# Optimization experiments

Hardware: AMD Instinct MI355X
Metric: run time of the kernel (lower is better)

Reference implementation:

```python
import jax, jax.numpy as jnp
import numpy as np

B, T, F, H = 1024, 128, 128, 256


def setup_inputs() -> dict:
    key = jax.random.key(0)
    ks = jax.random.split(key, 13)
    u = lambda k, shape, std: jax.random.uniform(k, shape, jnp.float32, -std, std)
    sH = 1.0 / np.sqrt(H)
    sF = 1.0 / np.sqrt(F)
    return {
        "X": jax.random.normal(ks[0], (B, T, F), jnp.float32),
        "M": (jax.random.uniform(ks[1], (B, T, F)) > 0.5).astype(jnp.float32),
        "Delta": jax.random.uniform(ks[2], (B, T, F), jnp.float32),
        "mu": jax.random.normal(ks[3], (B, 1, F), jnp.float32),
        "X_locf": jax.random.normal(ks[4], (B, T, F), jnp.float32),
        # TemporalDecay decay_h: W [H, F], b [H]
        "Wdh": u(ks[5], (H, F), sH),
        "bdh": u(ks[6], (H,), sH),
        # TemporalDecay decay_x (diag): W [F, F], b [F] (only diagonal of W used)
        "Wdx": u(ks[7], (F, F), sF),
        "bdx": u(ks[8], (F,), sF),
        # GRUCell: input size 2F+H, hidden H
        "Wih": u(ks[9], (3 * H, 2 * F + H), sH),
        "Whh": u(ks[10], (3 * H, H), sH),
        "bih": u(ks[11], (3 * H,), sH),
        "bhh": u(ks[12], (3 * H,), sH),
    }


def reference(X, M, Delta, mu, X_locf, Wdh, bdh, Wdx, bdx, Wih, Whh, bih, bhh):
    diag_x = jnp.diagonal(Wdx)  # diag=True: F.linear(d, W*I) == d * diag(W)
    mu_b = mu[:, 0, :]  # [B, F]

    def step(h, xs):
        x_t, m_t, d_t, xl_t = xs  # each [B, F]
        gamma_h = jnp.exp(-jax.nn.relu(d_t @ Wdh.T + bdh))  # [B, H]
        gamma_x = jnp.exp(-jax.nn.relu(d_t * diag_x + bdx))  # [B, F]
        h = h * gamma_h
        rep = h  # appended BEFORE the GRU cell update
        x_h = gamma_x * xl_t + (1.0 - gamma_x) * mu_b
        x_in = m_t * x_t + (1.0 - m_t) * x_h
        inp = jnp.concatenate([x_in, h, m_t], axis=1)  # [B, 2F+H]
        gi = inp @ Wih.T + bih
        gh = h @ Whh.T + bhh
        i_r, i_z, i_n = jnp.split(gi, 3, axis=1)
        h_r, h_z, h_n = jnp.split(gh, 3, axis=1)
        r = jax.nn.sigmoid(i_r + h_r)
        z = jax.nn.sigmoid(i_z + h_z)
        n = jnp.tanh(i_n + r * h_n)
        h_new = (1.0 - z) * n + z * h
        return h_new, rep

    xs = (jnp.swapaxes(X, 0, 1), jnp.swapaxes(M, 0, 1),
          jnp.swapaxes(Delta, 0, 1), jnp.swapaxes(X_locf, 0, 1))  # [T, B, F]
    h0 = jnp.zeros((X.shape[0], Whh.shape[1]), X.dtype)
    h_final, reps = jax.lax.scan(step, h0, xs)
    return jnp.swapaxes(reps, 0, 1), h_final  # ([B, T, H], [B, H])
```

## Files before the change

### kernel.cpp

```cpp
#include <hip/hip_runtime.h>
#include <cstdint>
#include <cstddef>

typedef __attribute__((ext_vector_type(8))) __bf16 bf16x8;
typedef __attribute__((ext_vector_type(8))) unsigned short u16x8;
typedef __attribute__((ext_vector_type(4))) unsigned short u16x4;
typedef __attribute__((ext_vector_type(2))) unsigned short u16x2;
typedef __attribute__((ext_vector_type(4))) float f32x4;
typedef __attribute__((ext_vector_type(2))) float f32x2;

__device__ __forceinline__ unsigned short f2bf(float f){
  unsigned int u = __float_as_uint(f);
  u += 0x7FFFu + ((u >> 16) & 1u);
  return (unsigned short)(u >> 16);
}
__device__ __forceinline__ float bf2f(unsigned short s){
  return __uint_as_float(((unsigned int)s) << 16);
}
__device__ __forceinline__ float sigm(float x){ return 1.f/(1.f + __expf(-x)); }
__device__ __forceinline__ float tanh_f(float x){ float e = __expf(2.f*x); return 1.f - 2.f/(e + 1.f); }
__device__ __forceinline__ f32x4 mfma16(u16x8 a, u16x8 b, f32x4 c){
  return __builtin_amdgcn_mfma_f32_16x16x32_bf16(
      __builtin_bit_cast(bf16x8, a), __builtin_bit_cast(bf16x8, b), c, 0, 0, 0);
}


__device__ __forceinline__ float wcval(int g, int n, int k,
    const float* __restrict__ Wih, const float* __restrict__ Whh){
  if (g==0) return Wih[n*512 + 128+k]       + Whh[n*256 + k];
  if (g==1) return Wih[(256+n)*512 + 128+k] + Whh[(256+n)*256 + k];
  if (g==2) return Wih[(512+n)*512 + 128+k];
  return Whh[(512+n)*256 + k];
}

__global__ __launch_bounds__(256) void kw(
    const float* __restrict__ Wdh, const float* __restrict__ Wih,
    const float* __restrict__ Whh, const float* __restrict__ bih,
    const float* __restrict__ bhh,
    unsigned short* __restrict__ WstrG, unsigned short* __restrict__ WldsG,
    unsigned short* __restrict__ W2,
    unsigned short* __restrict__ Wd, float* __restrict__ b2){
  int i0 = blockIdx.x*256 + threadIdx.x;
  int stride = gridDim.x*256;
  for (int idx=i0; idx<196608; idx+=stride){
    int j=idx&7, l=(idx>>3)&63, r=idx>>9;
    int i=r&7, r2=r>>3;
    int s=r2%6, w=r2/6;
    int ks = (s<4) ? s : (s+2);
    int g=i>>1, c=i&1;
    int n = (w*2+c)*16 + (l&15);
    int k = ks*32 + ((l>>4)<<3) + j;
    WstrG[idx] = f2bf(wcval(g, n, k, Wih, Whh));
  }
  for (int idx=i0; idx<65536; idx+=stride){
    int j=idx&7, l=(idx>>3)&63, r=idx>>9;
    int ks2=r&1, r2=r>>1;
    int c=r2&1, g=(r2>>1)&3, w=r2>>3;
    int n = (w*2+c)*16 + (l&15);
    int k = (4+ks2)*32 + ((l>>4)<<3) + j;
    WldsG[idx] = f2bf(wcval(g, n, k, Wih, Whh));
  }
  for (int idx=i0; idx<196608; idx+=stride){
    int j=idx&7, l=(idx>>3)&63, ks=(idx>>9)&7, nt=idx>>12;
    int n = nt*16 + (l&15);
    int k = ks*32 + ((l>>4)<<3) + j;
    float v = (k<128) ? Wih[n*512 + k] : Wih[n*512 + 256 + k];
    W2[idx] = f2bf(v);
  }
  for (int idx=i0; idx<32768; idx+=stride){
    int j=idx&7, l=(idx>>3)&63, ks=(idx>>9)&3, nt=idx>>11;
    int n = nt*16 + (l&15);
    int k = ks*32 + ((l>>4)<<3) + j;
    Wd[idx] = f2bf(Wdh[n*128 + k]);
  }
  for (int idx=i0; idx<768; idx+=stride)
    b2[idx] = bih[idx] + (idx<512 ? bhh[idx] : 0.f);
}

__global__ __launch_bounds__(256) void kprep(
    const float* __restrict__ X, const float* __restrict__ M,
    const float* __restrict__ D, const float* __restrict__ mu,
    const float* __restrict__ Xl, const float* __restrict__ Wdx,
    const float* __restrict__ bdx,
    unsigned short* __restrict__ Apre, unsigned short* __restrict__ Dt){
  int lane = threadIdx.x & 63;
  int wave = (blockIdx.x*256 + threadIdx.x) >> 6;
  int c0 = lane*2;
  float dg0 = Wdx[c0*128 + c0];
  float dg1 = Wdx[(c0+1)*128 + (c0+1)];
  float bx0 = bdx[c0], bx1 = bdx[c0+1];
  for (int r = wave; r < 131072; r += 4096){
    int t = r>>10, b = r&1023;
    size_t src = ((size_t)b*128 + t)*128 + c0;
    f32x2 x  = *(const f32x2*)(X+src);
    f32x2 m  = *(const f32x2*)(M+src);
    f32x2 d  = *(const f32x2*)(D+src);
    f32x2 xl = *(const f32x2*)(Xl+src);
    f32x2 mb = *(const f32x2*)(mu + b*128 + c0);
    float g0 = __expf(-fmaxf(0.f, d.x*dg0 + bx0));
    float g1 = __expf(-fmaxf(0.f, d.y*dg1 + bx1));
    float xh0 = g0*xl.x + (1.f-g0)*mb.x;
    float xh1 = g1*xl.y + (1.f-g1)*mb.y;
    float xi0 = m.x*x.x + (1.f-m.x)*xh0;
    float xi1 = m.y*x.y + (1.f-m.y)*xh1;
    size_t ar = (size_t)r*256;
    *(u16x2*)(Apre + ar + c0)        = u16x2{f2bf(xi0), f2bf(xi1)};
    *(u16x2*)(Apre + ar + 128 + c0)  = u16x2{f2bf(m.x), f2bf(m.y)};
    *(u16x2*)(Dt + (size_t)r*128 + c0) = u16x2{f2bf(d.x), f2bf(d.y)};
  }
}

template<int KS, int NTOT, int PNT, int MODE>
__global__ __launch_bounds__(512) void gemm_lds(
    const unsigned short* __restrict__ A, const unsigned short* __restrict__ Bw,
    const float* __restrict__ bias, unsigned short* __restrict__ out){
  extern __shared__ char smem[];
  unsigned short* Bs = (unsigned short*)smem;
  const int N = NTOT*16;
  const int lane = threadIdx.x & 63;
  const int w    = threadIdx.x >> 6;
  const size_t rb = (size_t)blockIdx.x*128 + w*16;
  const int lr = lane&15, lk=(lane>>4)<<3, lq=(lane>>4)<<2;
  u16x8 a[KS];
  #pragma unroll
  for (int ks=0; ks<KS; ++ks)
    a[ks] = *(const u16x8*)&A[(rb + lr)*(KS*32) + ks*32 + lk];
  #pragma unroll
  for (int p=0; p<NTOT/PNT; ++p){
    __syncthreads();
    {
      const u16x8* src = (const u16x8*)&Bw[(size_t)p*PNT*KS*512];
      u16x8* dst = (u16x8*)Bs;
      #pragma unroll
      for (int i=0; i<8; ++i)
        dst[threadIdx.x + i*512] = src[threadIdx.x + i*512];
    }
    __syncthreads();
    f32x4 acc[PNT];
    #pragma unroll
    for (int i=0; i<PNT; ++i) acc[i] = f32x4{0.f,0.f,0.f,0.f};
    #pragma unroll
    for (int ks=0; ks<KS; ++ks)
      #pragma unroll
      for (int i=0; i<PNT; ++i){
        u16x8 b = *(const u16x8*)&Bs[((i*KS + ks)*64 + lane)*8];
        acc[i] = mfma16(a[ks], b, acc[i]);
      }
    #pragma unroll
    for (int i=0; i<PNT; ++i){
      int col = (p*PNT + i)*16 + lr;
      float bv = bias[col];
      #pragma unroll
      for (int q=0; q<4; ++q){
        float v = acc[i][q] + bv;
        if (MODE==1) v = __expf(-fmaxf(0.f, v));
        out[(rb + lq + q)*(size_t)N + col] = f2bf(v);
      }
    }
  }
}

__global__ __launch_bounds__(512)
__attribute__((amdgpu_waves_per_eu(2, 2)))
void seq12(
    const unsigned short* __restrict__ WstrG, const unsigned short* __restrict__ WldsG,
    const unsigned short* __restrict__ gamma, const unsigned short* __restrict__ gipre,
    const float* __restrict__ bhh, float* __restrict__ out){
  extern __shared__ char smem[];
  unsigned short* Wlds = (unsigned short*)smem;
  unsigned short* hsw  = (unsigned short*)(smem + 131072);
  const int tid  = threadIdx.x;
  const int lane = tid & 63;
  const int w    = tid >> 6;
  const int bbase = blockIdx.x * 16;
  const int lr   = lane & 15;
  const int lq4  = (lane >> 4) << 2;

  for (int i = tid; i < 8192; i += 512)
    *(u16x8*)&Wlds[i*8] = *(const u16x8*)&WldsG[i*8];

  float h_reg[2][4];
  #pragma unroll
  for (int c=0; c<2; ++c)
    #pragma unroll
    for (int q=0; q<4; ++q) h_reg[c][q] = 0.f;

  float bnv[2];
  #pragma unroll
  for (int c=0; c<2; ++c) bnv[c] = bhh[512 + w*32 + c*16 + lr];

  unsigned short g_pre[2][4];
  #pragma unroll
  for (int c=0; c<2; ++c)
    #pragma unroll
    for (int q=0; q<4; ++q)
      g_pre[c][q] = gamma[((size_t)(bbase + lq4 + q))*256 + w*32 + c*16 + lr];

  const unsigned short* wsb = WstrG + (size_t)w*24576 + lane*8;

  __syncthreads();

  for (int t = 0; t < 128; ++t){
    #pragma unroll
    for (int c=0; c<2; ++c){
      const int col = w*32 + c*16 + lr;
      #pragma unroll
      for (int q=0; q<4; ++q){
        float hd = h_reg[c][q] * bf2f(g_pre[c][q]);
        h_reg[c][q] = hd;
        hsw[(col>>5)*512 + ((lq4+q) + (((col>>3)&3)<<4))*8 + (col&7)] = f2bf(hd);
      }
    }
    __syncthreads();

    #pragma unroll
    for (int c=0; c<2; ++c){
      const int col = w*32 + c*16 + lr;
      #pragma unroll
      for (int q=0; q<4; ++q)
        out[((size_t)(bbase+lq4+q)*128 + t)*256 + col] = h_reg[c][q];
    }

    f32x4 acc[4][2];
    #pragma unroll
    for (int g=0; g<4; ++g)
      #pragma unroll
      for (int c=0; c<2; ++c) acc[g][c] = f32x4{0.f,0.f,0.f,0.f};

    int off = 0;
    asm volatile("" : "+v"(off));
    const unsigned short* wp = wsb + off;

    u16x8 r0[8], r1[8], r2[8];
    #define ISS(r_, s_) { \
      _Pragma("unroll") \
      for (int i=0;i<8;++i) r_[i] = *(const u16x8*)(wp + ((s_)*8+i)*512); \
      } __builtin_amdgcn_sched_barrier(0);
    #define CONS(r_, ks_) { \
      u16x8 aR = *(const u16x8*)&hsw[(ks_)*512 + lane*8]; \
      _Pragma("unroll") \
      for (int i=0;i<8;++i) acc[i>>1][i&1] = mfma16(aR, r_[i], acc[i>>1][i&1]); \
      } __builtin_amdgcn_sched_barrier(0);

    ISS(r0,0) ISS(r1,1) ISS(r2,2)
    CONS(r0,0) ISS(r0,3)
    CONS(r1,1) ISS(r1,4)
    CONS(r2,2) ISS(r2,5)

    const unsigned short* gp = gipre + ((size_t)t*1024 + bbase)*768;
    unsigned short gv[3][2][4];
    #pragma unroll
    for (int g3=0; g3<3; ++g3)
      #pragma unroll
      for (int c=0; c<2; ++c)
        #pragma unroll
        for (int q=0; q<4; ++q)
          gv[g3][c][q] = gp[(size_t)(lq4+q)*768 + g3*256 + w*32 + c*16 + lr];
    if (t < 127){
      #pragma unroll
      for (int c=0; c<2; ++c)
        #pragma unroll
        for (int q=0; q<4; ++q)
          g_pre[c][q] = gamma[((size_t)(t+1)*1024 + bbase + lq4 + q)*256 + w*32 + c*16 + lr];
    }
    __builtin_amdgcn_sched_barrier(0);

    CONS(r0,3)
    #pragma unroll
    for (int ks2=0; ks2<2; ++ks2){
      u16x8 aL = *(const u16x8*)&hsw[(4+ks2)*512 + lane*8];
      #pragma unroll
      for (int g=0; g<4; ++g)
        #pragma unroll
        for (int c=0; c<2; ++c){
          u16x8 bL = *(const u16x8*)&Wlds[((w*8+g*2+c)*2 + ks2)*512 + lane*8];
          acc[g][c] = mfma16(aL, bL, acc[g][c]);
        }
    }
    __builtin_amdgcn_sched_barrier(0);
    CONS(r1,6)
    CONS(r2,7)
    #undef ISS
    #undef CONS
    __syncthreads();

    #pragma unroll
    for (int c=0; c<2; ++c){
      const int col = w*32 + c*16 + lr;
      #pragma unroll
      for (int q=0; q<4; ++q){
        float gr = bf2f(gv[0][c][q]);
        float gz = bf2f(gv[1][c][q]);
        float gn = bf2f(gv[2][c][q]);
        float rr = sigm(gr + acc[0][c][q]);
        float zz = sigm(gz + acc[1][c][q]);
        float nv = tanh_f(gn + acc[2][c][q] + rr*(acc[3][c][q] + bnv[c]));
        float hn = (1.f-zz)*nv + zz*h_reg[c][q];
        h_reg[c][q] = hn;
        if (t == 127) out[(size_t)33554432 + (size_t)(bbase+lq4+q)*256 + col] = hn;
      }
    }
  }
}

extern "C" void kernel_launch(void* const* d_in, const int* in_sizes, int n_in,
                              void* d_out, int out_size, void* d_ws, size_t ws_size,
                              hipStream_t stream){
  (void)in_sizes; (void)n_in; (void)out_size; (void)ws_size;
  const float* X   = (const float*)d_in[0];
  const float* M   = (const float*)d_in[1];
  const float* D   = (const float*)d_in[2];
  const float* mu  = (const float*)d_in[3];
  const float* Xl  = (const float*)d_in[4];
  const float* Wdh = (const float*)d_in[5];
  const float* bdh = (const float*)d_in[6];
  const float* Wdx = (const float*)d_in[7];
  const float* bdx = (const float*)d_in[8];
  const float* Wih = (const float*)d_in[9];
  const float* Whh = (const float*)d_in[10];
  const float* bih = (const float*)d_in[11];
  const float* bhh = (const float*)d_in[12];
  float* out = (float*)d_out;
  char* ws = (char*)d_ws;

  unsigned short* gipre = (unsigned short*)ws;
  unsigned short* gamma = (unsigned short*)(ws + 201326592);
  unsigned short* W2sw  = (unsigned short*)(ws + 268435456);
  unsigned short* Wdsw  = (unsigned short*)(ws + 268828672);
  unsigned short* WstrG = (unsigned short*)(ws + 268894208);
  unsigned short* WldsG = (unsigned short*)(ws + 269287424);
  float*          b2    = (float*)        (ws + 269418496);
  unsigned short* Apre = (unsigned short*)d_out;
  unsigned short* Dt   = (unsigned short*)((char*)d_out + 67108864);

  hipFuncSetAttribute(reinterpret_cast<const void*>(seq12),
                      hipFuncAttributeMaxDynamicSharedMemorySize, 139264);
  hipFuncSetAttribute(reinterpret_cast<const void*>(&gemm_lds<4,16,16,1>),
                      hipFuncAttributeMaxDynamicSharedMemorySize, 65536);
  hipFuncSetAttribute(reinterpret_cast<const void*>(&gemm_lds<8,48,8,0>),
                      hipFuncAttributeMaxDynamicSharedMemorySize, 65536);

  kw<<<256, 256, 0, stream>>>(Wdh, Wih, Whh, bih, bhh, WstrG, WldsG, W2sw, Wdsw, b2);
  kprep<<<1024, 256, 0, stream>>>(X, M, D, mu, Xl, Wdx, bdx, Apre, Dt);
  gemm_lds<4,16,16,1><<<1024, 512, 65536, stream>>>(Dt, Wdsw, bdh, gamma);
  gemm_lds<8,48,8,0><<<1024, 512, 65536, stream>>>(Apre, W2sw, b2, gipre);
  seq12<<<64, 512, 139264, stream>>>(WstrG, WldsG, gamma, gipre, bhh, out);
}
```

Baseline: 912.6 us.

## Split recurrent GRU step across 16 waves with one column tile each

The sequential GRU kernel now runs 1024 threads per block instead of 512, and each wave owns one 16-column tile of the hidden state instead of two. The weight pre-swizzle kernel is changed to match the new per-wave layout. Each wave then issues half as many MFMAs and weight loads per timestep, which shortens the serial per-step critical path. In exchange there are more waves meeting at each block barrier, and the old waves_per_eu hint is dropped, so register pressure and occupancy behaviour may change.

```diff
diff --git a/kernel.cpp b/kernel.cpp
--- a/kernel.cpp
+++ b/kernel.cpp
@@ -44,19 +44,17 @@
   int stride = gridDim.x*256;
   for (int idx=i0; idx<196608; idx+=stride){
     int j=idx&7, l=(idx>>3)&63, r=idx>>9;
-    int i=r&7, r2=r>>3;
+    int g=r&3, r2=r>>2;
     int s=r2%6, w=r2/6;
     int ks = (s<4) ? s : (s+2);
-    int g=i>>1, c=i&1;
-    int n = (w*2+c)*16 + (l&15);
+    int n = w*16 + (l&15);
     int k = ks*32 + ((l>>4)<<3) + j;
     WstrG[idx] = f2bf(wcval(g, n, k, Wih, Whh));
   }
   for (int idx=i0; idx<65536; idx+=stride){
     int j=idx&7, l=(idx>>3)&63, r=idx>>9;
-    int ks2=r&1, r2=r>>1;
-    int c=r2&1, g=(r2>>1)&3, w=r2>>3;
-    int n = (w*2+c)*16 + (l&15);
+    int ks2=r&1, g=(r>>1)&3, w=r>>3;
+    int n = w*16 + (l&15);
     int k = (4+ks2)*32 + ((l>>4)<<3) + j;
     WldsG[idx] = f2bf(wcval(g, n, k, Wih, Whh));
   }
@@ -160,9 +158,7 @@
   }
 }
 
-__global__ __launch_bounds__(512)
-__attribute__((amdgpu_waves_per_eu(2, 2)))
-void seq12(
+__global__ __launch_bounds__(1024) void seq13(
     const unsigned short* __restrict__ WstrG, const unsigned short* __restrict__ WldsG,
     const unsigned short* __restrict__ gamma, const unsigned short* __restrict__ gipre,
     const float* __restrict__ bhh, float* __restrict__ out){
@@ -175,71 +171,60 @@
   const int bbase = blockIdx.x * 16;
   const int lr   = lane & 15;
   const int lq4  = (lane >> 4) << 2;
-
-  for (int i = tid; i < 8192; i += 512)
+  const int col  = w*16 + lr;
+
+  for (int i = tid; i < 8192; i += 1024)
     *(u16x8*)&Wlds[i*8] = *(const u16x8*)&WldsG[i*8];
 
-  float h_reg[2][4];
-  #pragma unroll
-  for (int c=0; c<2; ++c)
-    #pragma unroll
-    for (int q=0; q<4; ++q) h_reg[c][q] = 0.f;
-
-  float bnv[2];
-  #pragma unroll
-  for (int c=0; c<2; ++c) bnv[c] = bhh[512 + w*32 + c*16 + lr];
-
-  unsigned short g_pre[2][4];
-  #pragma unroll
-  for (int c=0; c<2; ++c)
+  float h_reg[4];
+  #pragma unroll
+  for (int q=0; q<4; ++q) h_reg[q] = 0.f;
+  const float bnn = bhh[512 + col];
+
+  int sh[4];
+  #pragma unroll
+  for (int q=0; q<4; ++q)
+    sh[q] = (col>>5)*512 + ((lq4+q) + (((col>>3)&3)<<4))*8 + (col&7);
+
+  unsigned short g_pre[4];
+  #pragma unroll
+  for (int q=0; q<4; ++q)
+    g_pre[q] = gamma[((size_t)(bbase + lq4 + q))*256 + col];
+
+  const unsigned short* wsb = WstrG + (size_t)w*12288 + lane*8;
+
+  __syncthreads();
+
+  for (int t = 0; t < 128; ++t){
+    #pragma unroll
+    for (int q=0; q<4; ++q){
+      float hd = h_reg[q] * bf2f(g_pre[q]);
+      h_reg[q] = hd;
+      hsw[sh[q]] = f2bf(hd);
+    }
+    __syncthreads();
+
     #pragma unroll
     for (int q=0; q<4; ++q)
-      g_pre[c][q] = gamma[((size_t)(bbase + lq4 + q))*256 + w*32 + c*16 + lr];
-
-  const unsigned short* wsb = WstrG + (size_t)w*24576 + lane*8;
-
-  __syncthreads();
-
-  for (int t = 0; t < 128; ++t){
-    #pragma unroll
-    for (int c=0; c<2; ++c){
-      const int col = w*32 + c*16 + lr;
-      #pragma unroll
-      for (int q=0; q<4; ++q){
-        float hd = h_reg[c][q] * bf2f(g_pre[c][q]);
-        h_reg[c][q] = hd;
-        hsw[(col>>5)*512 + ((lq4+q) + (((col>>3)&3)<<4))*8 + (col&7)] = f2bf(hd);
-      }
-    }
-    __syncthreads();
-
-    #pragma unroll
-    for (int c=0; c<2; ++c){
-      const int col = w*32 + c*16 + lr;
-      #pragma unroll
-      for (int q=0; q<4; ++q)
-        out[((size_t)(bbase+lq4+q)*128 + t)*256 + col] = h_reg[c][q];
-    }
-
-    f32x4 acc[4][2];
-    #pragma unroll
-    for (int g=0; g<4; ++g)
-      #pragma unroll
-      for (int c=0; c<2; ++c) acc[g][c] = f32x4{0.f,0.f,0.f,0.f};
+      out[((size_t)(bbase+lq4+q)*128 + t)*256 + col] = h_reg[q];
+
+    f32x4 acc[4];
+    #pragma unroll
+    for (int g=0; g<4; ++g) acc[g] = f32x4{0.f,0.f,0.f,0.f};
 
     int off = 0;
     asm volatile("" : "+v"(off));
     const unsigned short* wp = wsb + off;
 
-    u16x8 r0[8], r1[8], r2[8];
+    u16x8 r0[4], r1[4], r2[4];
     #define ISS(r_, s_) { \
       _Pragma("unroll") \
-      for (int i=0;i<8;++i) r_[i] = *(const u16x8*)(wp + ((s_)*8+i)*512); \
+      for (int i=0;i<4;++i) r_[i] = *(const u16x8*)(wp + ((s_)*4+i)*512); \
       } __builtin_amdgcn_sched_barrier(0);
     #define CONS(r_, ks_) { \
       u16x8 aR = *(const u16x8*)&hsw[(ks_)*512 + lane*8]; \
       _Pragma("unroll") \
-      for (int i=0;i<8;++i) acc[i>>1][i&1] = mfma16(aR, r_[i], acc[i>>1][i&1]); \
+      for (int i=0;i<4;++i) acc[i] = mfma16(aR, r_[i], acc[i]); \
       } __builtin_amdgcn_sched_barrier(0);
 
     ISS(r0,0) ISS(r1,1) ISS(r2,2)
@@ -248,20 +233,16 @@
     CONS(r2,2) ISS(r2,5)
 
     const unsigned short* gp = gipre + ((size_t)t*1024 + bbase)*768;
-    unsigned short gv[3][2][4];
+    unsigned short gv[3][4];
     #pragma unroll
     for (int g3=0; g3<3; ++g3)
       #pragma unroll
-      for (int c=0; c<2; ++c)
-        #pragma unroll
-        for (int q=0; q<4; ++q)
-          gv[g3][c][q] = gp[(size_t)(lq4+q)*768 + g3*256 + w*32 + c*16 + lr];
+      for (int q=0; q<4; ++q)
+        gv[g3][q] = gp[(size_t)(lq4+q)*768 + g3*256 + col];
     if (t < 127){
       #pragma unroll
-      for (int c=0; c<2; ++c)
-        #pragma unroll
-        for (int q=0; q<4; ++q)
-          g_pre[c][q] = gamma[((size_t)(t+1)*1024 + bbase + lq4 + q)*256 + w*32 + c*16 + lr];
+      for (int q=0; q<4; ++q)
+        g_pre[q] = gamma[((size_t)(t+1)*1024 + bbase + lq4 + q)*256 + col];
     }
     __builtin_amdgcn_sched_barrier(0);
 
@@ -270,12 +251,10 @@
     for (int ks2=0; ks2<2; ++ks2){
       u16x8 aL = *(const u16x8*)&hsw[(4+ks2)*512 + lane*8];
       #pragma unroll
-      for (int g=0; g<4; ++g)
-        #pragma unroll
-        for (int c=0; c<2; ++c){
-          u16x8 bL = *(const u16x8*)&Wlds[((w*8+g*2+c)*2 + ks2)*512 + lane*8];
-          acc[g][c] = mfma16(aL, bL, acc[g][c]);
-        }
+      for (int g=0; g<4; ++g){
+        u16x8 bL = *(const u16x8*)&Wlds[((w*8 + g*2 + ks2)*64 + lane)*8];
+        acc[g] = mfma16(aL, bL, acc[g]);
+      }
     }
     __builtin_amdgcn_sched_barrier(0);
     CONS(r1,6)
@@ -285,20 +264,16 @@
     __syncthreads();
 
     #pragma unroll
-    for (int c=0; c<2; ++c){
-      const int col = w*32 + c*16 + lr;
-      #pragma unroll
-      for (int q=0; q<4; ++q){
-        float gr = bf2f(gv[0][c][q]);
-        float gz = bf2f(gv[1][c][q]);
-        float gn = bf2f(gv[2][c][q]);
-        float rr = sigm(gr + acc[0][c][q]);
-        float zz = sigm(gz + acc[1][c][q]);
-        float nv = tanh_f(gn + acc[2][c][q] + rr*(acc[3][c][q] + bnv[c]));
-        float hn = (1.f-zz)*nv + zz*h_reg[c][q];
-        h_reg[c][q] = hn;
-        if (t == 127) out[(size_t)33554432 + (size_t)(bbase+lq4+q)*256 + col] = hn;
-      }
+    for (int q=0; q<4; ++q){
+      float gr = bf2f(gv[0][q]);
+      float gz = bf2f(gv[1][q]);
+      float gn = bf2f(gv[2][q]);
+      float rr = sigm(gr + acc[0][q]);
+      float zz = sigm(gz + acc[1][q]);
+      float nv = tanh_f(gn + acc[2][q] + rr*(acc[3][q] + bnn));
+      float hn = (1.f-zz)*nv + zz*h_reg[q];
+      h_reg[q] = hn;
+      if (t == 127) out[(size_t)33554432 + (size_t)(bbase+lq4+q)*256 + col] = hn;
     }
   }
 }
@@ -333,7 +308,7 @@
   unsigned short* Apre = (unsigned short*)d_out;
   unsigned short* Dt   = (unsigned short*)((char*)d_out + 67108864);
 
-  hipFuncSetAttribute(reinterpret_cast<const void*>(seq12),
+  hipFuncSetAttribute(reinterpret_cast<const void*>(seq13),
                       hipFuncAttributeMaxDynamicSharedMemorySize, 139264);
   hipFuncSetAttribute(reinterpret_cast<const void*>(&gemm_lds<4,16,16,1>),
                       hipFuncAttributeMaxDynamicSharedMemorySize, 65536);
@@ -344,5 +319,5 @@
   kprep<<<1024, 256, 0, stream>>>(X, M, D, mu, Xl, Wdx, bdx, Apre, Dt);
   gemm_lds<4,16,16,1><<<1024, 512, 65536, stream>>>(Dt, Wdsw, bdh, gamma);
   gemm_lds<8,48,8,0><<<1024, 512, 65536, stream>>>(Apre, W2sw, b2, gipre);
-  seq12<<<64, 512, 139264, stream>>>(WstrG, WldsG, gamma, gipre, bhh, out);
-}
+  seq13<<<64, 1024, 139264, stream>>>(WstrG, WldsG, gamma, gipre, bhh, out);
+}
```

Result: no change. 922.7 us (+1.1%).
